# Kernel tuning notes

Hardware: AMD Instinct MI355X
Metric: run time of the kernel (lower is better)

## Reference

```python
import jax, jax.numpy as jnp
import numpy as np

SQRT2 = 1.4142135623730951

def _oyzx2spin():
    # 0yzx -> (uu, ud, du, dd) spin projection matrix, complex64
    M = np.array([[1, 0, 1, 0],
                  [0, -1j, 0, 1],
                  [0, 1j, 0, 1],
                  [1, 0, -1, 0]], dtype=np.complex64) / SQRT2
    return jnp.asarray(M)


def setup_inputs() -> dict:
    key = jax.random.key(0)
    B, C_real, nL, nR = 65536, 8, 13, 13  # C_real = 2 * C_complex (soc_complex_doubling), C_complex % 4 == 0
    HR_in = jax.random.normal(key, (B, C_real, nL, nR), dtype=jnp.float32)
    return {"HR_in": HR_in}


def reference(HR_in):
    # Faithful translation of E3Hamiltonian._spin_projection with
    # real storage + soc_complex_doubling=True.
    B, C_real, nL, nR = HR_in.shape
    half = C_real // 2  # complex channel count
    # pack complex-doubled real storage into complex channels
    HR_c = jax.lax.complex(HR_in[:, :half], HR_in[:, half:])  # [B, half, nL, nR] complex
    n_chunks = half // 4
    HR_view = HR_c.reshape(B, n_chunks, 4, nL, nR)  # 4 = (0, y, z, x) spin components
    M = _oyzx2spin()  # [4(spin), 4(0yzx)]
    # project 0yzx components onto (uu, ud, du, dd) spin basis
    HR_proj = jnp.einsum('nkslr,ps->nkplr', HR_view, M)
    HR_proj_flat = HR_proj.reshape(B, half, nL, nR)
    # unpack back to real storage: [real-half | imag-half] along channel dim
    return jnp.concatenate([HR_proj_flat.real, HR_proj_flat.imag], axis=1)
```

## Files before the change

### kernel.cpp

```cpp
#include <hip/hip_runtime.h>


#define PLANE 169
#define CSTRIDE 1352
#define CHUNKS 43
#define PPI 4

typedef float f4u __attribute__((ext_vector_type(4), aligned(4)));

__global__ __launch_bounds__(256) void spin_proj_kernel(
    const float* __restrict__ in, float* __restrict__ out, int total) {
    int t = blockIdx.x * blockDim.x + threadIdx.x;
    if (t >= total) return;

    int n = t / (PPI * CHUNKS);
    int r = t - n * (PPI * CHUNKS);
    int p = r / CHUNKS;
    int k = r - p * CHUNKS;

    int sh = p * 4;
    int A  = (0x7430 >> sh) & 0xF;
    int B  = (0x1652 >> sh) & 0xF;
    int CU = (0x6410 >> sh) & 0xF;
    int CW = (0x5723 >> sh) & 0xF;

    const float s = 0.70710678118654752440f;
    size_t base = (size_t)n * CSTRIDE;
    const float* __restrict__ ia = in  + base + A  * PLANE;
    const float* __restrict__ ib = in  + base + B  * PLANE;
    float* __restrict__ oa       = out + base + CU * PLANE;
    float* __restrict__ ob       = out + base + CW * PLANE;

    if (k < 42) {
        int j = 4 * k;
        f4u x = *(const f4u*)(ia + j);
        f4u y = *(const f4u*)(ib + j);
        f4u u = (x + y) * s;
        f4u w = (x - y) * s;
        *(f4u*)(oa + j) = u;
        *(f4u*)(ob + j) = w;
    } else {
        float x = ia[168];
        float y = ib[168];
        oa[168] = (x + y) * s;
        ob[168] = (x - y) * s;
    }
}

extern "C" void kernel_launch(void* const* d_in, const int* in_sizes, int n_in,
                              void* d_out, int out_size, void* d_ws, size_t ws_size,
                              hipStream_t stream) {
    const float* in = (const float*)d_in[0];
    float* out = (float*)d_out;

    int n_items = in_sizes[0] / CSTRIDE;
    int total = n_items * PPI * CHUNKS;
    int grid = (total + 255) / 256;
    spin_proj_kernel<<<grid, 256, 0, stream>>>(in, out, total);
}
```

Before: 142.6 us.

## Make each thread write one contiguous aligned float4 of output

Each thread now owns four consecutive output floats rather than one plane pair, so stores become fully coalesced, 16-byte-aligned float4 writes, since CSTRIDE is a multiple of 4. The thread gathers its two source planes, which are selected through packed lookup constants with sign-encoded coefficients, and combines them with an FMA. Quads that cross a plane boundary fall back to scalar gathers. The cost is that input loads may be misaligned and are read twice across threads, and there is some extra index arithmetic.

```diff
diff --git a/kernel.cpp b/kernel.cpp
--- a/kernel.cpp
+++ b/kernel.cpp
@@ -3,48 +3,62 @@
 
 #define PLANE 169
 #define CSTRIDE 1352
-#define CHUNKS 43
-#define PPI 4
+#define QPI 338
 
 typedef float f4u __attribute__((ext_vector_type(4), aligned(4)));
 
+__device__ __forceinline__ float mix_one(const float* __restrict__ ib,
+                                         int c, int j) {
+    const int A = (0x41140330u >> (c * 4)) & 0xF;
+    const int B = (0x67762552u >> (c * 4)) & 0xF;
+    const unsigned ca_bits = 0x3F3504F3u | (((0x20u >> c) & 1u) << 31);
+    const unsigned cb_bits = 0x3F3504F3u | (((0x8Cu >> c) & 1u) << 31);
+    float v = ib[A * PLANE + j] * __builtin_bit_cast(float, ca_bits);
+    return fmaf(ib[B * PLANE + j], __builtin_bit_cast(float, cb_bits), v);
+}
+
 __global__ __launch_bounds__(256) void spin_proj_kernel(
     const float* __restrict__ in, float* __restrict__ out, int total) {
-    int t = blockIdx.x * blockDim.x + threadIdx.x;
+    int t = blockIdx.x * 256 + threadIdx.x;
     if (t >= total) return;
 
-    int n = t / (PPI * CHUNKS);
-    int r = t - n * (PPI * CHUNKS);
-    int p = r / CHUNKS;
-    int k = r - p * CHUNKS;
+    const int n = t / QPI;
+    const int q = t - n * QPI;
+    const int idx0 = 4 * q;
+    const int c0 = idx0 / PLANE;
+    const int j0 = idx0 - c0 * PLANE;
 
-    int sh = p * 4;
-    int A  = (0x7430 >> sh) & 0xF;
-    int B  = (0x1652 >> sh) & 0xF;
-    int CU = (0x6410 >> sh) & 0xF;
-    int CW = (0x5723 >> sh) & 0xF;
+    const float* __restrict__ ib = in + (size_t)n * CSTRIDE;
+    float4 o;
 
-    const float s = 0.70710678118654752440f;
-    size_t base = (size_t)n * CSTRIDE;
-    const float* __restrict__ ia = in  + base + A  * PLANE;
-    const float* __restrict__ ib = in  + base + B  * PLANE;
-    float* __restrict__ oa       = out + base + CU * PLANE;
-    float* __restrict__ ob       = out + base + CW * PLANE;
+    if (j0 <= PLANE - 4) {
+        const int A = (0x41140330u >> (c0 * 4)) & 0xF;
+        const int B = (0x67762552u >> (c0 * 4)) & 0xF;
+        const unsigned ca_bits = 0x3F3504F3u | (((0x20u >> c0) & 1u) << 31);
+        const unsigned cb_bits = 0x3F3504F3u | (((0x8Cu >> c0) & 1u) << 31);
+        const float ca = __builtin_bit_cast(float, ca_bits);
+        const float cb = __builtin_bit_cast(float, cb_bits);
+        f4u x = *(const f4u*)(ib + A * PLANE + j0);
+        f4u y = *(const f4u*)(ib + B * PLANE + j0);
+        o.x = fmaf(y.x, cb, x.x * ca);
+        o.y = fmaf(y.y, cb, x.y * ca);
+        o.z = fmaf(y.z, cb, x.z * ca);
+        o.w = fmaf(y.w, cb, x.w * ca);
+    } else {
+        int cA = c0,     jA = j0;
+        int cB = c0,     jB = j0 + 1;
+        int cC = c0,     jC = j0 + 2;
+        int cD = c0,     jD = j0 + 3;
+        if (jB >= PLANE) { cB++; jB -= PLANE; }
+        if (jC >= PLANE) { cC++; jC -= PLANE; }
+        if (jD >= PLANE) { cD++; jD -= PLANE; }
+        o.x = mix_one(ib, cA, jA);
+        o.y = mix_one(ib, cB, jB);
+        o.z = mix_one(ib, cC, jC);
+        o.w = mix_one(ib, cD, jD);
+    }
 
-    if (k < 42) {
-        int j = 4 * k;
-        f4u x = *(const f4u*)(ia + j);
-        f4u y = *(const f4u*)(ib + j);
-        f4u u = (x + y) * s;
-        f4u w = (x - y) * s;
-        *(f4u*)(oa + j) = u;
-        *(f4u*)(ob + j) = w;
-    } else {
-        float x = ia[168];
-        float y = ib[168];
-        oa[168] = (x + y) * s;
-        ob[168] = (x - y) * s;
-    }
+    *(float4*)(out + (size_t)n * CSTRIDE + idx0) = o;
 }
 
 extern "C" void kernel_launch(void* const* d_in, const int* in_sizes, int n_in,
@@ -53,8 +67,8 @@
     const float* in = (const float*)d_in[0];
     float* out = (float*)d_out;
 
-    int n_items = in_sizes[0] / CSTRIDE;
-    int total = n_items * PPI * CHUNKS;
-    int grid = (total + 255) / 256;
+    const int n_items = in_sizes[0] / CSTRIDE;
+    const int total = n_items * QPI;
+    const int grid = (total + 255) / 256;
     spin_proj_kernel<<<grid, 256, 0, stream>>>(in, out, total);
 }
```

Result: faster. 132.7 us (-6.9%).
